# Kernel optimization log

Measured on AMD Instinct MI355X. Metric: run time of the kernel, lower is better.

The kernel has to match this reference:

```python
import jax, jax.numpy as jnp
import numpy as np

N_ENT = 200000   # n_entities
N_NODES = 20000  # nodes in subgraph
N_EDGES = 320000 # avg degree 16
R = 40           # n_relations
B = 34           # num_bases (hard-coded in module)
D_IN = 128       # emb_dim_init
D_HID = 128      # hidden_dim
D_OUT = 128      # out_dim


def setup_inputs() -> dict:
    key = jax.random.key(0)
    ks = jax.random.split(key, 14)
    s = 0.05
    return {
        "node_index": jax.random.randint(ks[0], (N_NODES,), 0, N_ENT),
        "edge_index": jax.random.randint(ks[1], (2, N_EDGES), 0, N_NODES),
        "edge_type": jax.random.randint(ks[2], (N_EDGES,), 0, R),
        "node_frequency": jax.random.normal(ks[3], (N_NODES,), jnp.float32),
        "node_emb": jax.random.normal(ks[4], (N_ENT, D_IN), jnp.float32),
        "comp0": jax.random.normal(ks[5], (R, B), jnp.float32) * s,
        "bases0": jax.random.normal(ks[6], (B, D_IN, D_HID), jnp.float32) * s,
        "root0": jax.random.normal(ks[7], (D_IN, D_HID), jnp.float32) * s,
        "bias0": jnp.zeros((D_HID,), jnp.float32),
        "comp1": jax.random.normal(ks[8], (R, B), jnp.float32) * s,
        "bases1": jax.random.normal(ks[9], (B, D_HID, D_OUT), jnp.float32) * s,
        "root1": jax.random.normal(ks[10], (D_HID, D_OUT), jnp.float32) * s,
        "bias1": jnp.zeros((D_OUT,), jnp.float32),
    }


def _rgcn_conv(x, src, dst, etype, comp, bases, root, bias):
    """Basis-decomposed RGCNConv (PyG semantics: per-relation mean aggregation
    over incoming edges, plus root transform and bias)."""
    n = x.shape[0]
    # relation weights from basis decomposition: [R, in, out]
    W = jnp.einsum('rb,bio->rio', comp, bases)
    # transform all nodes by every relation weight: [R, N, out]
    h_all = jnp.einsum('ni,rio->rno', x, W)
    # gather per-edge message x[src] @ W[edge_type]: [E, out]
    msg = h_all[etype, src]
    # mean-aggregate per (dst node, relation) segment
    seg = dst * R + etype
    sums = jax.ops.segment_sum(msg, seg, num_segments=n * R)  # [N*R, out]
    cnt = jax.ops.segment_sum(jnp.ones((msg.shape[0],), x.dtype), seg,
                              num_segments=n * R)
    mean = sums / jnp.maximum(cnt, 1.0)[:, None]
    agg = mean.reshape(n, R, -1).sum(axis=1)  # sum over relations: [N, out]
    return agg + x @ root + bias


def reference(node_index, edge_index, edge_type, node_frequency, node_emb,
              comp0, bases0, root0, bias0, comp1, bases1, root1, bias1):
    # node_frequency is accepted but unused (matches original forward).
    x = node_emb[node_index]                      # [N, D_IN]
    src, dst = edge_index[0], edge_index[1]
    x = _rgcn_conv(x, src, dst, edge_type, comp0, bases0, root0, bias0)
    x = _rgcn_conv(x, src, dst, edge_type, comp1, bases1, root1, bias1)
    return x
```

## Files before the change

kernel.cpp:

```cpp
#include <hip/hip_runtime.h>

#define N_NODES  20000
#define N_EDGES  320000
#define R_REL    40
#define N_BASES  34
#define DIM      128
#define EB       128
#define P_PAD    (N_EDGES + R_REL * EB)
#define ROOT_PAD ((N_NODES + EB - 1) / EB * EB)
#define P2_MAX   (P_PAD + ROOT_PAD)
#define NE2      (N_EDGES + N_NODES)

typedef unsigned int uint;
typedef unsigned short ushort;
typedef __attribute__((ext_vector_type(8))) short short8;
typedef __attribute__((ext_vector_type(4))) float f32x4;

__device__ __forceinline__ ushort f2bf(float f) {
    uint u = __float_as_uint(f);
    return (ushort)((u + 0x7FFFu + ((u >> 16) & 1u)) >> 16);
}
__device__ __forceinline__ uint pk2bf(float a, float b) {
    return (uint)f2bf(a) | ((uint)f2bf(b) << 16);
}

__global__ void init_kernel(int* __restrict__ c_cnt, int* __restrict__ meta_cur2_deg,
                            uint4* __restrict__ esrc) {
    int i = blockIdx.x * blockDim.x + threadIdx.x;
    if (i < N_NODES * R_REL) c_cnt[i] = 0;
    if (i < P2_MAX) esrc[i] = make_uint4((uint)-1, (uint)-1, 0u, 0u);
    if (i < 256 + 2 * N_NODES) meta_cur2_deg[i] = 0;
}

__global__ void count_kernel(const int* __restrict__ ei, const int* __restrict__ et,
                             int* __restrict__ c, int* __restrict__ h,
                             int* __restrict__ deg) {
    __shared__ int hloc[R_REL];
    int t = threadIdx.x;
    if (t < R_REL) hloc[t] = 0;
    __syncthreads();
    int e = blockIdx.x * blockDim.x + t;
    if (e < N_EDGES) {
        int dst = ei[N_EDGES + e];
        int r   = et[e];
        atomicAdd(&c[dst * R_REL + r], 1);
        atomicAdd(&deg[dst], 1);
        atomicAdd(&hloc[r], 1);
    }
    __syncthreads();
    if (t < R_REL && hloc[t]) atomicAdd(&h[t], hloc[t]);
}

__global__ void inv_kernel(const int* __restrict__ c, float* __restrict__ finv) {
    int i = blockIdx.x * blockDim.x + threadIdx.x;
    if (i < N_NODES * R_REL) {
        int v = c[i];
        finv[i] = 1.0f / (float)(v < 1 ? 1 : v);
    }
}

__global__ void scans_kernel(const int* __restrict__ deg, const int* __restrict__ h,
                             int* __restrict__ ptr, int* __restrict__ off) {
    __shared__ int part[256];
    const int CHn = (N_NODES + 255) / 256;
    int t = threadIdx.x;
    int s = 0;
    for (int i = 0; i < CHn; ++i) {
        int idx = t * CHn + i;
        if (idx < N_NODES) s += deg[idx] + 1;
    }
    part[t] = s;
    __syncthreads();
    for (int d = 1; d < 256; d <<= 1) {
        int v = (t >= d) ? part[t - d] : 0;
        __syncthreads();
        part[t] += v;
        __syncthreads();
    }
    int base = (t > 0) ? part[t - 1] : 0;
    for (int i = 0; i < CHn; ++i) {
        int idx = t * CHn + i;
        if (idx < N_NODES) { ptr[idx] = base; base += deg[idx] + 1; }
    }
    if (t == 0) {
        ptr[N_NODES] = NE2;
        int acc = 0;
        off[0] = 0;
        for (int r = 0; r < R_REL; ++r) {
            acc += ((h[r] + EB - 1) / EB) * EB;
            off[r + 1] = acc;
        }
        off[R_REL + 1] = acc + ROOT_PAD;
    }
}

__global__ void place_kernel(const int* __restrict__ ei, const int* __restrict__ et,
                             const int* __restrict__ off, int* __restrict__ cur,
                             const float* __restrict__ finv,
                             const int* __restrict__ ptr, int* __restrict__ cur2,
                             uint4* __restrict__ esrc) {
    __shared__ int hloc[R_REL];
    __shared__ int base[R_REL];
    int t = threadIdx.x;
    if (t < R_REL) hloc[t] = 0;
    __syncthreads();
    int e = blockIdx.x * blockDim.x + t;
    int r = 0, myrank = 0, src = 0, dst = 0;
    bool isEdge = (e < N_EDGES);
    if (isEdge) {
        r = et[e]; src = ei[e]; dst = ei[N_EDGES + e];
        myrank = atomicAdd(&hloc[r], 1);
    }
    __syncthreads();
    if (t < R_REL) base[t] = hloc[t] ? atomicAdd(&cur[t], hloc[t]) : 0;
    __syncthreads();
    if (isEdge) {
        int p = off[r] + base[r] + myrank;
        int q = ptr[dst] + 1 + atomicAdd(&cur2[dst], 1);
        esrc[p] = make_uint4((uint)src, (uint)q,
                             __float_as_uint(finv[dst * R_REL + r]), 0u);
    } else if (e < N_EDGES + N_NODES) {
        int n = e - N_EDGES;
        esrc[off[R_REL] + n] = make_uint4((uint)n, (uint)ptr[n], 0x3f800000u, 0u);
    }
}

__global__ void gather_bf16_kernel(const float* __restrict__ emb, const int* __restrict__ idx,
                                   ushort* __restrict__ xb) {
    int t = blockIdx.x * blockDim.x + threadIdx.x;
    int n = t >> 4, v = t & 15;
    const float4* s = (const float4*)(emb + (size_t)idx[n] * DIM + v * 8);
    float4 a = s[0], b = s[1];
    uint4 o;
    o.x = pk2bf(a.x, a.y); o.y = pk2bf(a.z, a.w);
    o.z = pk2bf(b.x, b.y); o.w = pk2bf(b.z, b.w);
    *(uint4*)(xb + (size_t)n * DIM + v * 8) = o;
}

__global__ void wtrans_kernel(const float* __restrict__ comp, const float* __restrict__ bases,
                              const float* __restrict__ root, ushort* __restrict__ Wt) {
    __shared__ float tile[32][33];
    __shared__ float scomp[N_BASES];
    int slot = blockIdx.x >> 4;
    int tb   = blockIdx.x & 15;
    int k0 = (tb >> 2) * 32, n0 = (tb & 3) * 32;
    int t = threadIdx.x, tr = t >> 5, tc = t & 31;
    if (slot < R_REL) {
        if (t < N_BASES) scomp[t] = comp[slot * N_BASES + t];
        __syncthreads();
        #pragma unroll
        for (int i = 0; i < 4; ++i) {
            int kk = tr + 8 * i;
            float acc = 0.f;
            #pragma unroll
            for (int b = 0; b < N_BASES; ++b)
                acc += scomp[b] * bases[((size_t)b * DIM + k0 + kk) * DIM + n0 + tc];
            tile[kk][tc] = acc;
        }
    } else {
        #pragma unroll
        for (int i = 0; i < 4; ++i) {
            int kk = tr + 8 * i;
            tile[kk][tc] = root[(size_t)(k0 + kk) * DIM + n0 + tc];
        }
    }
    __syncthreads();
    #pragma unroll
    for (int i = 0; i < 4; ++i) {
        int rr = tr + 8 * i;
        Wt[(size_t)slot * DIM * DIM + (size_t)(n0 + rr) * DIM + k0 + tc] = f2bf(tile[tc][rr]);
    }
}

__launch_bounds__(256)
__global__ void edge_mfma_kernel(const uint4* __restrict__ esrc, const int* __restrict__ off,
                                 const ushort* __restrict__ xb, const ushort* __restrict__ Wt,
                                 ushort* __restrict__ T) {
    __shared__ __align__(16) ushort Ws[DIM * DIM];
    __shared__ int soff[R_REL + 2];
    int t = threadIdx.x;
    if (t < R_REL + 2) soff[t] = off[t];
    __syncthreads();
    int e0 = blockIdx.x * EB;
    if (e0 >= soff[R_REL + 1]) return;
    int r = 0;
    while (e0 >= soff[r + 1]) ++r;

    const ushort* Wr = Wt + (size_t)r * DIM * DIM;
    #pragma unroll
    for (int i = 0; i < 8; ++i) {
        int idx = t + 256 * i;
        int row = idx >> 4, slot = idx & 15;
        uint4 v = *(const uint4*)(Wr + row * DIM + slot * 8);
        *(uint4*)(&Ws[row * DIM + ((slot ^ (row & 15)) * 8)]) = v;
    }
    __syncthreads();

    int wv = t >> 6;
    int l  = t & 63;
    int lr = l & 15;
    int lk = l >> 4;

    int er0 = e0 + wv * 32 + lr;
    int er1 = er0 + 16;
    uint4 es0 = esrc[er0], es1 = esrc[er1];
    int s0 = (int)es0.x, q0 = (int)es0.y;
    int s1 = (int)es1.x, q1 = (int)es1.y;
    float esc0 = __uint_as_float(es0.z), esc1 = __uint_as_float(es1.z);
    const ushort* x0p = xb + (size_t)(s0 < 0 ? 0 : s0) * DIM;
    const ushort* x1p = xb + (size_t)(s1 < 0 ? 0 : s1) * DIM;

    short8 xf0[4], xf1[4];
    #pragma unroll
    for (int ks = 0; ks < 4; ++ks) {
        xf0[ks] = *(const short8*)(x0p + (ks * 4 + lk) * 8);
        xf1[ks] = *(const short8*)(x1p + (ks * 4 + lk) * 8);
    }

    f32x4 acc0[8], acc1[8];
    #pragma unroll
    for (int mt = 0; mt < 8; ++mt) { acc0[mt] = (f32x4){0.f,0.f,0.f,0.f}; acc1[mt] = (f32x4){0.f,0.f,0.f,0.f}; }

    #pragma unroll
    for (int ks = 0; ks < 4; ++ks) {
        #pragma unroll
        for (int mt = 0; mt < 8; ++mt) {
            int row = mt * 16 + lr;
            int slot = (ks * 4 + lk) ^ lr;
            short8 wf = *(const short8*)(&Ws[row * DIM + slot * 8]);
            acc0[mt] = __builtin_amdgcn_mfma_f32_16x16x32_bf16(wf, xf0[ks], acc0[mt], 0, 0, 0);
            acc1[mt] = __builtin_amdgcn_mfma_f32_16x16x32_bf16(wf, xf1[ks], acc1[mt], 0, 0, 0);
        }
    }

    ushort* T0 = T + (size_t)q0 * DIM;
    ushort* T1 = T + (size_t)q1 * DIM;
    #pragma unroll
    for (int mt = 0; mt < 8; ++mt) {
        if (q0 >= 0) {
            uint2 p0;
            p0.x = pk2bf(acc0[mt][0] * esc0, acc0[mt][1] * esc0);
            p0.y = pk2bf(acc0[mt][2] * esc0, acc0[mt][3] * esc0);
            *(uint2*)(T0 + mt * 16 + lk * 4) = p0;
        }
        if (q1 >= 0) {
            uint2 p1;
            p1.x = pk2bf(acc1[mt][0] * esc1, acc1[mt][1] * esc1);
            p1.y = pk2bf(acc1[mt][2] * esc1, acc1[mt][3] * esc1);
            *(uint2*)(T1 + mt * 16 + lk * 4) = p1;
        }
    }
}

template<int OUT_BF16>
__global__ void aggregate_kernel(const int* __restrict__ ptr, const ushort* __restrict__ T,
                                 const float* __restrict__ bias, void* __restrict__ yout) {
    int n = blockIdx.x;
    int t = threadIdx.x;
    int s0 = ptr[n], s1 = ptr[n + 1];
    float a0 = bias[2 * t], a1 = bias[2 * t + 1];
    for (int q = s0; q < s1; ++q) {
        uint v = *(const uint*)(T + (size_t)q * DIM + 2 * t);
        a0 += __uint_as_float(v << 16);
        a1 += __uint_as_float(v & 0xFFFF0000u);
    }
    if (OUT_BF16) {
        ((uint*)yout)[n * 64 + t] = pk2bf(a0, a1);
    } else {
        ((float2*)yout)[n * 64 + t] = make_float2(a0, a1);
    }
}

extern "C" void kernel_launch(void* const* d_in, const int* in_sizes, int n_in,
                              void* d_out, int out_size, void* d_ws, size_t ws_size,
                              hipStream_t stream) {
    const int*   node_index = (const int*)d_in[0];
    const int*   edge_index = (const int*)d_in[1];
    const int*   edge_type  = (const int*)d_in[2];
    const float* node_emb   = (const float*)d_in[4];
    const float* comp0  = (const float*)d_in[5];
    const float* bases0 = (const float*)d_in[6];
    const float* root0  = (const float*)d_in[7];
    const float* bias0  = (const float*)d_in[8];
    const float* comp1  = (const float*)d_in[9];
    const float* bases1 = (const float*)d_in[10];
    const float* root1  = (const float*)d_in[11];
    const float* bias1  = (const float*)d_in[12];
    float* out = (float*)d_out;

    char* ws = (char*)d_ws;
    int*    c_cnt  = (int*)   (ws);
    float*  finv   = (float*) (ws +  3200000);
    ushort* Wt     = (ushort*)(ws +  6400000);
    ushort* x0b    = (ushort*)(ws +  7743488);
    ushort* y0b    = (ushort*)(ws + 12863488);
    uint4*  esrc   = (uint4*) (ws + 17983488);
    int*    meta   = (int*)   (ws + 23506944);
    int*    cur2   = (int*)   (ws + 23507968);
    int*    deg    = (int*)   (ws + 23587968);
    int*    ptr    = (int*)   (ws + 23667968);
    ushort* T      = (ushort*)(ws + 23748480);
    int* off = meta;
    int* h   = meta + 64;
    int* cur = meta + 128;

    init_kernel<<<(N_NODES * R_REL + 255) / 256, 256, 0, stream>>>(c_cnt, meta, esrc);
    count_kernel<<<(N_EDGES + 255) / 256, 256, 0, stream>>>(edge_index, edge_type, c_cnt, h, deg);
    inv_kernel<<<(N_NODES * R_REL + 255) / 256, 256, 0, stream>>>(c_cnt, finv);
    scans_kernel<<<1, 256, 0, stream>>>(deg, h, ptr, off);
    place_kernel<<<(N_EDGES + N_NODES + 255) / 256, 256, 0, stream>>>(
        edge_index, edge_type, off, cur, finv, ptr, cur2, esrc);
    gather_bf16_kernel<<<N_NODES * 16 / 256, 256, 0, stream>>>(node_emb, node_index, x0b);

    const int wtBlocks = (R_REL + 1) * 16;
    const int eBlocks  = P2_MAX / EB;

    wtrans_kernel<<<wtBlocks, 256, 0, stream>>>(comp0, bases0, root0, Wt);
    edge_mfma_kernel<<<eBlocks, 256, 0, stream>>>(esrc, off, x0b, Wt, T);
    aggregate_kernel<1><<<N_NODES, 64, 0, stream>>>(ptr, T, bias0, y0b);

    wtrans_kernel<<<wtBlocks, 256, 0, stream>>>(comp1, bases1, root1, Wt);
    edge_mfma_kernel<<<eBlocks, 256, 0, stream>>>(esrc, off, y0b, Wt, T);
    aggregate_kernel<0><<<N_NODES, 64, 0, stream>>>(ptr, T, bias1, out);
}
```

Baseline: 285.2 us.

## Merge weight transforms, drop inv kernel, persist edge blocks per relation

Removes the separate reciprocal-count kernel and computes 1/count inline in place_kernel. Both layers' weight transforms now run in one launch. The edge MFMA kernel now uses a fixed grid of 32 blocks per relation slot, each looping over 128-edge chunks, so the 32 KB W tile is loaded into LDS once per block instead of once per chunk. Aggregation packs two nodes per block and the scan uses 1024 threads. The fixed grid risks load imbalance and lower occupancy, since only 41×32 blocks run and the root slot has many more chunks than the relation slots.

```diff
diff --git a/kernel.cpp b/kernel.cpp
--- a/kernel.cpp
+++ b/kernel.cpp
@@ -10,6 +10,7 @@
 #define ROOT_PAD ((N_NODES + EB - 1) / EB * EB)
 #define P2_MAX   (P_PAD + ROOT_PAD)
 #define NE2      (N_EDGES + N_NODES)
+#define NSLOT    (R_REL + 1)
 
 typedef unsigned int uint;
 typedef unsigned short ushort;
@@ -51,18 +52,10 @@
     if (t < R_REL && hloc[t]) atomicAdd(&h[t], hloc[t]);
 }
 
-__global__ void inv_kernel(const int* __restrict__ c, float* __restrict__ finv) {
-    int i = blockIdx.x * blockDim.x + threadIdx.x;
-    if (i < N_NODES * R_REL) {
-        int v = c[i];
-        finv[i] = 1.0f / (float)(v < 1 ? 1 : v);
-    }
-}
-
 __global__ void scans_kernel(const int* __restrict__ deg, const int* __restrict__ h,
                              int* __restrict__ ptr, int* __restrict__ off) {
-    __shared__ int part[256];
-    const int CHn = (N_NODES + 255) / 256;
+    __shared__ int part[1024];
+    const int CHn = (N_NODES + 1023) / 1024;
     int t = threadIdx.x;
     int s = 0;
     for (int i = 0; i < CHn; ++i) {
@@ -71,7 +64,7 @@
     }
     part[t] = s;
     __syncthreads();
-    for (int d = 1; d < 256; d <<= 1) {
+    for (int d = 1; d < 1024; d <<= 1) {
         int v = (t >= d) ? part[t - d] : 0;
         __syncthreads();
         part[t] += v;
@@ -96,7 +89,7 @@
 
 __global__ void place_kernel(const int* __restrict__ ei, const int* __restrict__ et,
                              const int* __restrict__ off, int* __restrict__ cur,
-                             const float* __restrict__ finv,
+                             const int* __restrict__ c_cnt,
                              const int* __restrict__ ptr, int* __restrict__ cur2,
                              uint4* __restrict__ esrc) {
     __shared__ int hloc[R_REL];
@@ -117,8 +110,9 @@
     if (isEdge) {
         int p = off[r] + base[r] + myrank;
         int q = ptr[dst] + 1 + atomicAdd(&cur2[dst], 1);
-        esrc[p] = make_uint4((uint)src, (uint)q,
-                             __float_as_uint(finv[dst * R_REL + r]), 0u);
+        int cnt = c_cnt[dst * R_REL + r];
+        float esc = 1.0f / (float)(cnt < 1 ? 1 : cnt);
+        esrc[p] = make_uint4((uint)src, (uint)q, __float_as_uint(esc), 0u);
     } else if (e < N_EDGES + N_NODES) {
         int n = e - N_EDGES;
         esrc[off[R_REL] + n] = make_uint4((uint)n, (uint)ptr[n], 0x3f800000u, 0u);
@@ -137,12 +131,21 @@
     *(uint4*)(xb + (size_t)n * DIM + v * 8) = o;
 }
 
-__global__ void wtrans_kernel(const float* __restrict__ comp, const float* __restrict__ bases,
-                              const float* __restrict__ root, ushort* __restrict__ Wt) {
+__global__ void wtrans_kernel(const float* __restrict__ comp0, const float* __restrict__ bases0,
+                              const float* __restrict__ root0,
+                              const float* __restrict__ comp1, const float* __restrict__ bases1,
+                              const float* __restrict__ root1,
+                              ushort* __restrict__ Wt) {
     __shared__ float tile[32][33];
     __shared__ float scomp[N_BASES];
-    int slot = blockIdx.x >> 4;
-    int tb   = blockIdx.x & 15;
+    int b = blockIdx.x;
+    int layer = (b >= NSLOT * 16) ? 1 : 0;
+    int bb = b - layer * NSLOT * 16;
+    const float* comp  = layer ? comp1  : comp0;
+    const float* bases = layer ? bases1 : bases0;
+    const float* root  = layer ? root1  : root0;
+    int slot = bb >> 4;
+    int tb   = bb & 15;
     int k0 = (tb >> 2) * 32, n0 = (tb & 3) * 32;
     int t = threadIdx.x, tr = t >> 5, tc = t & 31;
     if (slot < R_REL) {
@@ -153,8 +156,8 @@
             int kk = tr + 8 * i;
             float acc = 0.f;
             #pragma unroll
-            for (int b = 0; b < N_BASES; ++b)
-                acc += scomp[b] * bases[((size_t)b * DIM + k0 + kk) * DIM + n0 + tc];
+            for (int bs = 0; bs < N_BASES; ++bs)
+                acc += scomp[bs] * bases[((size_t)bs * DIM + k0 + kk) * DIM + n0 + tc];
             tile[kk][tc] = acc;
         }
     } else {
@@ -165,26 +168,24 @@
         }
     }
     __syncthreads();
+    size_t obase = ((size_t)layer * NSLOT + slot) * DIM * DIM;
     #pragma unroll
     for (int i = 0; i < 4; ++i) {
         int rr = tr + 8 * i;
-        Wt[(size_t)slot * DIM * DIM + (size_t)(n0 + rr) * DIM + k0 + tc] = f2bf(tile[tc][rr]);
-    }
-}
-
+        Wt[obase + (size_t)(n0 + rr) * DIM + k0 + tc] = f2bf(tile[tc][rr]);
+    }
+}
+
+#define SUBS 32
 __launch_bounds__(256)
 __global__ void edge_mfma_kernel(const uint4* __restrict__ esrc, const int* __restrict__ off,
                                  const ushort* __restrict__ xb, const ushort* __restrict__ Wt,
                                  ushort* __restrict__ T) {
     __shared__ __align__(16) ushort Ws[DIM * DIM];
-    __shared__ int soff[R_REL + 2];
-    int t = threadIdx.x;
-    if (t < R_REL + 2) soff[t] = off[t];
-    __syncthreads();
-    int e0 = blockIdx.x * EB;
-    if (e0 >= soff[R_REL + 1]) return;
-    int r = 0;
-    while (e0 >= soff[r + 1]) ++r;
+    int t = threadIdx.x;
+    int r   = blockIdx.x >> 5;
+    int sub = blockIdx.x & (SUBS - 1);
+    int s_lo = off[r], s_hi = off[r + 1];
 
     const ushort* Wr = Wt + (size_t)r * DIM * DIM;
     #pragma unroll
@@ -201,53 +202,60 @@
     int lr = l & 15;
     int lk = l >> 4;
 
-    int er0 = e0 + wv * 32 + lr;
-    int er1 = er0 + 16;
-    uint4 es0 = esrc[er0], es1 = esrc[er1];
-    int s0 = (int)es0.x, q0 = (int)es0.y;
-    int s1 = (int)es1.x, q1 = (int)es1.y;
-    float esc0 = __uint_as_float(es0.z), esc1 = __uint_as_float(es1.z);
-    const ushort* x0p = xb + (size_t)(s0 < 0 ? 0 : s0) * DIM;
-    const ushort* x1p = xb + (size_t)(s1 < 0 ? 0 : s1) * DIM;
-
-    short8 xf0[4], xf1[4];
-    #pragma unroll
-    for (int ks = 0; ks < 4; ++ks) {
-        xf0[ks] = *(const short8*)(x0p + (ks * 4 + lk) * 8);
-        xf1[ks] = *(const short8*)(x1p + (ks * 4 + lk) * 8);
-    }
-
-    f32x4 acc0[8], acc1[8];
-    #pragma unroll
-    for (int mt = 0; mt < 8; ++mt) { acc0[mt] = (f32x4){0.f,0.f,0.f,0.f}; acc1[mt] = (f32x4){0.f,0.f,0.f,0.f}; }
-
-    #pragma unroll
-    for (int ks = 0; ks < 4; ++ks) {
+    int nch = (s_hi - s_lo) >> 7;
+    for (int c = sub; c < nch; c += SUBS) {
+        int e0 = s_lo + (c << 7);
+        int er0 = e0 + wv * 32 + lr;
+        int er1 = er0 + 16;
+        uint4 es0 = esrc[er0], es1 = esrc[er1];
+        int s0 = (int)es0.x, q0 = (int)es0.y;
+        int s1 = (int)es1.x, q1 = (int)es1.y;
+        float esc0 = __uint_as_float(es0.z), esc1 = __uint_as_float(es1.z);
+        const ushort* x0p = xb + (size_t)(s0 < 0 ? 0 : s0) * DIM;
+        const ushort* x1p = xb + (size_t)(s1 < 0 ? 0 : s1) * DIM;
+
+        short8 xf0[4], xf1[4];
+        #pragma unroll
+        for (int ks = 0; ks < 4; ++ks) {
+            xf0[ks] = *(const short8*)(x0p + (ks * 4 + lk) * 8);
+            xf1[ks] = *(const short8*)(x1p + (ks * 4 + lk) * 8);
+        }
+
+        f32x4 acc0[8], acc1[8];
         #pragma unroll
         for (int mt = 0; mt < 8; ++mt) {
-            int row = mt * 16 + lr;
-            int slot = (ks * 4 + lk) ^ lr;
-            short8 wf = *(const short8*)(&Ws[row * DIM + slot * 8]);
-            acc0[mt] = __builtin_amdgcn_mfma_f32_16x16x32_bf16(wf, xf0[ks], acc0[mt], 0, 0, 0);
-            acc1[mt] = __builtin_amdgcn_mfma_f32_16x16x32_bf16(wf, xf1[ks], acc1[mt], 0, 0, 0);
-        }
-    }
-
-    ushort* T0 = T + (size_t)q0 * DIM;
-    ushort* T1 = T + (size_t)q1 * DIM;
-    #pragma unroll
-    for (int mt = 0; mt < 8; ++mt) {
-        if (q0 >= 0) {
-            uint2 p0;
-            p0.x = pk2bf(acc0[mt][0] * esc0, acc0[mt][1] * esc0);
-            p0.y = pk2bf(acc0[mt][2] * esc0, acc0[mt][3] * esc0);
-            *(uint2*)(T0 + mt * 16 + lk * 4) = p0;
-        }
-        if (q1 >= 0) {
-            uint2 p1;
-            p1.x = pk2bf(acc1[mt][0] * esc1, acc1[mt][1] * esc1);
-            p1.y = pk2bf(acc1[mt][2] * esc1, acc1[mt][3] * esc1);
-            *(uint2*)(T1 + mt * 16 + lk * 4) = p1;
+            acc0[mt] = (f32x4){0.f, 0.f, 0.f, 0.f};
+            acc1[mt] = (f32x4){0.f, 0.f, 0.f, 0.f};
+        }
+
+        #pragma unroll
+        for (int ks = 0; ks < 4; ++ks) {
+            #pragma unroll
+            for (int mt = 0; mt < 8; ++mt) {
+                int row = mt * 16 + lr;
+                int slot = (ks * 4 + lk) ^ lr;
+                short8 wf = *(const short8*)(&Ws[row * DIM + slot * 8]);
+                acc0[mt] = __builtin_amdgcn_mfma_f32_16x16x32_bf16(wf, xf0[ks], acc0[mt], 0, 0, 0);
+                acc1[mt] = __builtin_amdgcn_mfma_f32_16x16x32_bf16(wf, xf1[ks], acc1[mt], 0, 0, 0);
+            }
+        }
+
+        ushort* T0 = T + (size_t)q0 * DIM;
+        ushort* T1 = T + (size_t)q1 * DIM;
+        #pragma unroll
+        for (int mt = 0; mt < 8; ++mt) {
+            if (q0 >= 0) {
+                uint2 p0;
+                p0.x = pk2bf(acc0[mt][0] * esc0, acc0[mt][1] * esc0);
+                p0.y = pk2bf(acc0[mt][2] * esc0, acc0[mt][3] * esc0);
+                *(uint2*)(T0 + mt * 16 + lk * 4) = p0;
+            }
+            if (q1 >= 0) {
+                uint2 p1;
+                p1.x = pk2bf(acc1[mt][0] * esc1, acc1[mt][1] * esc1);
+                p1.y = pk2bf(acc1[mt][2] * esc1, acc1[mt][3] * esc1);
+                *(uint2*)(T1 + mt * 16 + lk * 4) = p1;
+            }
         }
     }
 }
@@ -255,19 +263,20 @@
 template<int OUT_BF16>
 __global__ void aggregate_kernel(const int* __restrict__ ptr, const ushort* __restrict__ T,
                                  const float* __restrict__ bias, void* __restrict__ yout) {
-    int n = blockIdx.x;
-    int t = threadIdx.x;
+    int t = threadIdx.x;
+    int n = blockIdx.x * 2 + (t >> 6);
+    int tt = t & 63;
     int s0 = ptr[n], s1 = ptr[n + 1];
-    float a0 = bias[2 * t], a1 = bias[2 * t + 1];
+    float a0 = bias[2 * tt], a1 = bias[2 * tt + 1];
     for (int q = s0; q < s1; ++q) {
-        uint v = *(const uint*)(T + (size_t)q * DIM + 2 * t);
+        uint v = *(const uint*)(T + (size_t)q * DIM + 2 * tt);
         a0 += __uint_as_float(v << 16);
         a1 += __uint_as_float(v & 0xFFFF0000u);
     }
     if (OUT_BF16) {
-        ((uint*)yout)[n * 64 + t] = pk2bf(a0, a1);
+        ((uint*)yout)[n * 64 + tt] = pk2bf(a0, a1);
     } else {
-        ((float2*)yout)[n * 64 + t] = make_float2(a0, a1);
+        ((float2*)yout)[n * 64 + tt] = make_float2(a0, a1);
     }
 }
 
@@ -290,36 +299,34 @@
 
     char* ws = (char*)d_ws;
     int*    c_cnt  = (int*)   (ws);
-    float*  finv   = (float*) (ws +  3200000);
-    ushort* Wt     = (ushort*)(ws +  6400000);
-    ushort* x0b    = (ushort*)(ws +  7743488);
-    ushort* y0b    = (ushort*)(ws + 12863488);
-    uint4*  esrc   = (uint4*) (ws + 17983488);
-    int*    meta   = (int*)   (ws + 23506944);
-    int*    cur2   = (int*)   (ws + 23507968);
-    int*    deg    = (int*)   (ws + 23587968);
-    int*    ptr    = (int*)   (ws + 23667968);
-    ushort* T      = (ushort*)(ws + 23748480);
+    ushort* Wt     = (ushort*)(ws +  3200000);
+    ushort* x0b    = (ushort*)(ws +  5886976);
+    ushort* y0b    = (ushort*)(ws + 11006976);
+    uint4*  esrc   = (uint4*) (ws + 16126976);
+    int*    meta   = (int*)   (ws + 21650432);
+    int*    cur2   = (int*)   (ws + 21651456);
+    int*    deg    = (int*)   (ws + 21731456);
+    int*    ptr    = (int*)   (ws + 21811456);
+    ushort* T      = (ushort*)(ws + 21891712);
     int* off = meta;
     int* h   = meta + 64;
     int* cur = meta + 128;
 
     init_kernel<<<(N_NODES * R_REL + 255) / 256, 256, 0, stream>>>(c_cnt, meta, esrc);
     count_kernel<<<(N_EDGES + 255) / 256, 256, 0, stream>>>(edge_index, edge_type, c_cnt, h, deg);
-    inv_kernel<<<(N_NODES * R_REL + 255) / 256, 256, 0, stream>>>(c_cnt, finv);
-    scans_kernel<<<1, 256, 0, stream>>>(deg, h, ptr, off);
+    scans_kernel<<<1, 1024, 0, stream>>>(deg, h, ptr, off);
     place_kernel<<<(N_EDGES + N_NODES + 255) / 256, 256, 0, stream>>>(
-        edge_index, edge_type, off, cur, finv, ptr, cur2, esrc);
+        edge_index, edge_type, off, cur, c_cnt, ptr, cur2, esrc);
     gather_bf16_kernel<<<N_NODES * 16 / 256, 256, 0, stream>>>(node_emb, node_index, x0b);
-
-    const int wtBlocks = (R_REL + 1) * 16;
-    const int eBlocks  = P2_MAX / EB;
-
-    wtrans_kernel<<<wtBlocks, 256, 0, stream>>>(comp0, bases0, root0, Wt);
+    wtrans_kernel<<<2 * NSLOT * 16, 256, 0, stream>>>(comp0, bases0, root0,
+                                                      comp1, bases1, root1, Wt);
+
+    const int eBlocks = NSLOT * SUBS;
+
     edge_mfma_kernel<<<eBlocks, 256, 0, stream>>>(esrc, off, x0b, Wt, T);
-    aggregate_kernel<1><<<N_NODES, 64, 0, stream>>>(ptr, T, bias0, y0b);
-
-    wtrans_kernel<<<wtBlocks, 256, 0, stream>>>(comp1, bases1, root1, Wt);
-    edge_mfma_kernel<<<eBlocks, 256, 0, stream>>>(esrc, off, y0b, Wt, T);
-    aggregate_kernel<0><<<N_NODES, 64, 0, stream>>>(ptr, T, bias1, out);
-}
+    aggregate_kernel<1><<<N_NODES / 2, 128, 0, stream>>>(ptr, T, bias0, y0b);
+
+    edge_mfma_kernel<<<eBlocks, 256, 0, stream>>>(esrc, off, y0b,
+                                                  Wt + (size_t)NSLOT * DIM * DIM, T);
+    aggregate_kernel<0><<<N_NODES / 2, 128, 0, stream>>>(ptr, T, bias1, out);
+}
```

Result: no change. 284.5 us (-0.3%).
